# Kernel tuning notes

Measured on AMD Instinct MI355X. Metric: run time of the kernel, lower is better.

Reference implementation:

```python
import jax, jax.numpy as jnp
import numpy as np

D_MODEL = 1024
NUM_HEADS = 16
D_K = D_MODEL // NUM_HEADS
SCALE = float(np.sqrt(D_K))
NEG_FILL = -10000.0


def setup_inputs() -> dict:
    key = jax.random.key(0)
    ks = jax.random.split(key, 12)
    B, S = 2, 2048
    q = jax.random.normal(ks[0], (B, S, D_MODEL), dtype=jnp.float32)
    k = jax.random.normal(ks[1], (B, S, D_MODEL), dtype=jnp.float32)
    v = jax.random.normal(ks[2], (B, S, D_MODEL), dtype=jnp.float32)
    mask = jnp.ones((B, S, S), dtype=bool)
    w = lambda kk: jax.random.normal(kk, (D_MODEL, D_MODEL), dtype=jnp.float32) * 0.02
    b = lambda kk: jax.random.normal(kk, (D_MODEL,), dtype=jnp.float32) * 0.02
    return {
        "q": q, "k": k, "v": v, "mask": mask,
        "Wq": w(ks[3]), "bq": b(ks[4]),
        "Wk": w(ks[5]), "bk": b(ks[6]),
        "Wv": w(ks[7]), "bv": b(ks[8]),
        "Wo": w(ks[9]), "bo": b(ks[10]),
    }


def _mha(q, k, v, mask, Wq, bq, Wk, bk, Wv, bv, Wo, bo):
    B, S, _ = q.shape
    # torch Linear: x @ W.T + b
    def proj(x, W, bias):
        y = x @ W.T + bias
        return y.reshape(B, -1, NUM_HEADS, D_K).transpose(0, 2, 1, 3)  # [B,H,S,d_k]
    qh = proj(q, Wq, bq)
    kh = proj(k, Wk, bk)
    vh = proj(v, Wv, bv)
    scores = jnp.einsum('bhqd,bhkd->bhqk', qh, kh) / SCALE  # [B,H,S,S]
    scores = jnp.where(mask[:, None, :, :], scores, NEG_FILL)
    attn = jax.nn.softmax(scores, axis=-1)
    # dropout p=0.0 (eval) -> identity
    out = jnp.einsum('bhqk,bhkd->bhqd', attn, vh)  # [B,H,S,d_k]
    out = out.transpose(0, 2, 1, 3).reshape(B, -1, D_MODEL)
    return out @ Wo.T + bo


def reference(q, k, v, mask, Wq, bq, Wk, bk, Wv, bv, Wo, bo):
    return _mha(q, k, v, mask, Wq, bq, Wk, bk, Wv, bv, Wo, bo)
```

## Files before the change

kernel.cpp:

```cpp
#include <hip/hip_runtime.h>
#include <hip/hip_bf16.h>
#include <stdint.h>


typedef __bf16 bf16x8 __attribute__((ext_vector_type(8)));
typedef float  f32x4  __attribute__((ext_vector_type(4)));

#define GLD16(gp, lp)                                                         \
  __builtin_amdgcn_global_load_lds(                                           \
      (const __attribute__((address_space(1))) void*)(gp),                    \
      (__attribute__((address_space(3))) void*)(lp), 16, 0, 0)

#if __has_builtin(__builtin_amdgcn_exp2f)
#define EXP2F(x) __builtin_amdgcn_exp2f(x)
#else
#define EXP2F(x) exp2f(x)
#endif

__device__ __forceinline__ unsigned short f2bu(float f) {
  __bf16 b = (__bf16)f;
  return __builtin_bit_cast(unsigned short, b);
}
__device__ __forceinline__ f32x4 mfma16(bf16x8 a, bf16x8 b, f32x4 c) {
  return __builtin_amdgcn_mfma_f32_16x16x32_bf16(a, b, c, 0, 0, 0);
}

template <int CTRL>
__device__ __forceinline__ float dppf(float x) {
  int r = __builtin_amdgcn_update_dpp(0, __builtin_bit_cast(int, x),
                                      CTRL, 0xF, 0xF, true);
  return __builtin_bit_cast(float, r);
}
__device__ __forceinline__ float rowmax16(float x) {
  x = fmaxf(x, dppf<0xB1>(x));
  x = fmaxf(x, dppf<0x4E>(x));
  x = fmaxf(x, dppf<0x124>(x));
  x = fmaxf(x, dppf<0x128>(x));
  return x;
}
__device__ __forceinline__ float rowsum16(float x) {
  x += dppf<0xB1>(x);
  x += dppf<0x4E>(x);
  x += dppf<0x124>(x);
  x += dppf<0x128>(x);
  return x;
}

#define Q_PRESCALE 0.18033688011117290f
#define RESCALE_THR 8.0f

__global__ __launch_bounds__(256) void convert_kernel(
    const float* __restrict__ q, const float* __restrict__ k,
    const float* __restrict__ v, const float* __restrict__ wq,
    const float* __restrict__ wk, const float* __restrict__ wv,
    const float* __restrict__ wo, unsigned short* __restrict__ xq,
    unsigned short* __restrict__ xk, unsigned short* __restrict__ xv,
    unsigned short* __restrict__ cwq, unsigned short* __restrict__ cwk,
    unsigned short* __restrict__ cwv, unsigned short* __restrict__ cwo) {
  const int seg = blockIdx.y;
  const float* src; unsigned short* dst; int n4;
  const int NB = 4194304 / 4, NW = 1048576 / 4;
  switch (seg) {
    case 0: src = q;  dst = xq;  n4 = NB; break;
    case 1: src = k;  dst = xk;  n4 = NB; break;
    case 2: src = v;  dst = xv;  n4 = NB; break;
    case 3: src = wq; dst = cwq; n4 = NW; break;
    case 4: src = wk; dst = cwk; n4 = NW; break;
    case 5: src = wv; dst = cwv; n4 = NW; break;
    default: src = wo; dst = cwo; n4 = NW; break;
  }
  const int stride = gridDim.x * blockDim.x;
  for (int i = blockIdx.x * blockDim.x + threadIdx.x; i < n4; i += stride) {
    float4 f = ((const float4*)src)[i];
    ushort4 o;
    o.x = f2bu(f.x); o.y = f2bu(f.y); o.z = f2bu(f.z); o.w = f2bu(f.w);
    ((ushort4*)dst)[i] = o;
  }
}

template <int FN>
__device__ __forceinline__ void gemm_tile_bt(
    const unsigned short* __restrict__ A, const unsigned short* __restrict__ B,
    int am0, int bn0, unsigned short* sA, unsigned short* sB,
    f32x4 (&acc)[4][FN]) {
  const int tid = threadIdx.x;
  const int l = tid & 63, w = tid >> 6;
  const int wr = w >> 1, wc = w & 1;
  const f32x4 z4 = {0.f, 0.f, 0.f, 0.f};
#pragma unroll
  for (int i = 0; i < 4; i++)
#pragma unroll
    for (int j = 0; j < FN; j++) acc[i][j] = z4;

  for (int kk = 0; kk < 1024; kk += 64) {
#pragma unroll
    for (int it = 0; it < 4; ++it) {
      int c = it * 256 + tid;
      int row = c >> 3, c8 = (c & 7) * 8;
      GLD16(A + (size_t)(am0 + row) * 1024 + kk + c8,
            sA + (size_t)(it * 256 + w * 64) * 8);
    }
#pragma unroll
    for (int it = 0; it < FN; ++it) {
      int c = it * 256 + tid;
      int row = c >> 3, c8 = (c & 7) * 8;
      GLD16(B + (size_t)(bn0 + row) * 1024 + kk + c8,
            sB + (size_t)(it * 256 + w * 64) * 8);
    }
    __syncthreads();
    bf16x8 af[4][2], bfr[FN][2];
#pragma unroll
    for (int fm = 0; fm < 4; fm++)
#pragma unroll
      for (int h = 0; h < 2; h++)
        af[fm][h] = *reinterpret_cast<const bf16x8*>(
            sA + (wr * 64 + fm * 16 + (l & 15)) * 64 + 8 * (l >> 4) + 32 * h);
#pragma unroll
    for (int fn = 0; fn < FN; fn++)
#pragma unroll
      for (int h = 0; h < 2; h++)
        bfr[fn][h] = *reinterpret_cast<const bf16x8*>(
            sB + (wc * (FN * 16) + fn * 16 + (l & 15)) * 64 + 8 * (l >> 4) +
            32 * h);
#pragma unroll
    for (int fm = 0; fm < 4; fm++)
#pragma unroll
      for (int fn = 0; fn < FN; fn++) {
        acc[fm][fn] = mfma16(af[fm][0], bfr[fn][0], acc[fm][fn]);
        acc[fm][fn] = mfma16(af[fm][1], bfr[fn][1], acc[fm][fn]);
      }
    __syncthreads();
  }
}

__global__ __launch_bounds__(256, 3) void gemm_proj(
    const unsigned short* __restrict__ Xq, const unsigned short* __restrict__ Xk,
    const unsigned short* __restrict__ Xv, const unsigned short* __restrict__ Wq,
    const unsigned short* __restrict__ Wk, const unsigned short* __restrict__ Wv,
    const float* __restrict__ bq, const float* __restrict__ bk,
    const float* __restrict__ bv, unsigned short* __restrict__ Qh,
    unsigned short* __restrict__ Kh, unsigned short* __restrict__ Vt) {
  __shared__ unsigned short sA[128 * 64], sB[128 * 64];
  const int z = blockIdx.z;
  const unsigned short* X = (z == 0) ? Xq : (z == 1) ? Xk : Xv;
  const unsigned short* W = (z == 0) ? Wq : (z == 1) ? Wk : Wv;
  const float* bias = (z == 0) ? bq : (z == 1) ? bk : bv;
  const float scale = (z == 0) ? Q_PRESCALE : 1.0f;
  const int am0 = blockIdx.x * 128, bn0 = blockIdx.y * 128;
  f32x4 acc[4][4];
  gemm_tile_bt<4>(X, W, am0, bn0, sA, sB, acc);
  const int l = threadIdx.x & 63, w = threadIdx.x >> 6;
  const int wr = w >> 1, wc = w & 1;
  if (z < 2) {
    unsigned short* out = (z == 0) ? Qh : Kh;
#pragma unroll
    for (int fm = 0; fm < 4; fm++)
#pragma unroll
      for (int fn = 0; fn < 4; fn++) {
        int n = bn0 + wc * 64 + fn * 16 + (l & 15);
        int hh = n >> 6, d = n & 63;
        float bb = bias[n];
#pragma unroll
        for (int r = 0; r < 4; r++) {
          int m = am0 + wr * 64 + fm * 16 + (l >> 4) * 4 + r;
          int bidx = m >> 11, s = m & 2047;
          out[(((size_t)(bidx * 16 + hh) * 2048 + s)) * 64 + d] =
              f2bu((acc[fm][fn][r] + bb) * scale);
        }
      }
  } else {
#pragma unroll
    for (int fm = 0; fm < 4; fm++)
#pragma unroll
      for (int fn = 0; fn < 4; fn++) {
        int n = bn0 + wc * 64 + fn * 16 + (l & 15);
        int hh = n >> 6, d = n & 63;
        float bb = bias[n];
        int m0 = am0 + wr * 64 + fm * 16 + (l >> 4) * 4;
        int bidx = m0 >> 11, s0 = m0 & 2047;
        ushort4 pk;
        pk.x = f2bu(acc[fm][fn][0] + bb);
        pk.y = f2bu(acc[fm][fn][1] + bb);
        pk.z = f2bu(acc[fm][fn][2] + bb);
        pk.w = f2bu(acc[fm][fn][3] + bb);
        *(ushort4*)(Vt + ((size_t)(bidx * 16 + hh) * 64 + d) * 2048 + s0) = pk;
      }
  }
}

__global__ __launch_bounds__(256, 4) void attn_kernel(
    const unsigned short* __restrict__ Qh, const unsigned short* __restrict__ Kh,
    const unsigned short* __restrict__ Vt, unsigned short* __restrict__ Oh) {
  __shared__ unsigned short Ks[2][64 * 64];
  __shared__ unsigned short Vs[2][64 * 64];
  __shared__ unsigned short Ps[4][16 * 64];
  const int tid = threadIdx.x, l = tid & 63, w = tid >> 6;
  const int lid = blockIdx.x + 32 * blockIdx.y + 512 * blockIdx.z;
  const int swz = (lid & 7) * 128 + (lid >> 3);
  const int qt = swz & 31, h = (swz >> 5) & 15, b = swz >> 9;
  const size_t headoff = ((size_t)b * 16 + h) * 2048 * 64;
  const unsigned short* Qg = Qh + headoff + (size_t)(qt * 64 + w * 16) * 64;
  const unsigned short* Kg = Kh + headoff;
  const unsigned short* Vg = Vt + headoff;
  unsigned short* Pw = &Ps[w][0];

  bf16x8 qf[2];
#pragma unroll
  for (int hh = 0; hh < 2; hh++)
    qf[hh] = *reinterpret_cast<const bf16x8*>(
        Qg + (l & 15) * 64 + 8 * (l >> 4) + 32 * hh);

  float mrow[4], lrow[4];
  f32x4 oacc[4];
  const f32x4 z4 = {0.f, 0.f, 0.f, 0.f};
#pragma unroll
  for (int r = 0; r < 4; r++) { mrow[r] = -1e30f; lrow[r] = 0.f; }
#pragma unroll
  for (int fn = 0; fn < 4; fn++) oacc[fn] = z4;

  const int xoro[2] = { (((l >> 4) + 0) ^ (l & 7)) * 8,
                        (((l >> 4) + 4) ^ (l & 7)) * 8 };
  const int rowb = (l & 15) * 64;

#define STAGE_KV(dst, kt_)                                                    \
  do {                                                                        \
    _Pragma("unroll")                                                         \
    for (int it = 0; it < 2; ++it) {                                          \
      int c = it * 256 + tid;                                                 \
      int row = c >> 3;                                                       \
      int sc = (((c & 7) ^ (row & 7)) * 8);                                   \
      GLD16(Kg + (size_t)((kt_) * 64 + row) * 64 + sc,                        \
            &Ks[dst][0] + (size_t)(it * 256 + w * 64) * 8);                   \
      GLD16(Vg + (size_t)row * 2048 + (kt_) * 64 + sc,                        \
            &Vs[dst][0] + (size_t)(it * 256 + w * 64) * 8);                   \
    }                                                                         \
  } while (0)

  STAGE_KV(0, 0);
  __syncthreads();

#pragma unroll 2
  for (int kt = 0; kt < 32; ++kt) {
    const int cur = kt & 1;
    if (kt + 1 < 32) STAGE_KV(cur ^ 1, kt + 1);

    bf16x8 kf[4][2];
#pragma unroll
    for (int fn = 0; fn < 4; fn++)
#pragma unroll
      for (int hh = 0; hh < 2; hh++)
        kf[fn][hh] = *reinterpret_cast<const bf16x8*>(
            &Ks[cur][0] + fn * 1024 + rowb + xoro[hh]);
    f32x4 sfr[4];
#pragma unroll
    for (int fn = 0; fn < 4; fn++) {
      f32x4 sc = z4;
      sc = mfma16(qf[0], kf[fn][0], sc);
      sc = mfma16(qf[1], kf[fn][1], sc);
      sfr[fn] = sc;
    }

    float tmv[4];
    bool needb = false;
#pragma unroll
    for (int r = 0; r < 4; r++) {
      float tm = fmaxf(fmaxf(sfr[0][r], sfr[1][r]),
                       fmaxf(sfr[2][r], sfr[3][r]));
      tm = rowmax16(tm);
      tmv[r] = tm;
      needb = needb || (tm > mrow[r] + RESCALE_THR);
    }
    if (__any(needb)) {
#pragma unroll
      for (int r = 0; r < 4; r++) {
        float newm = fmaxf(mrow[r], tmv[r]);
        float corr = EXP2F(mrow[r] - newm);
        mrow[r] = newm;
        float rs = 0.f;
#pragma unroll
        for (int fn = 0; fn < 4; fn++) {
          float p = EXP2F(sfr[fn][r] - newm);
          sfr[fn][r] = p;
          rs += p;
        }
        rs = rowsum16(rs);
        lrow[r] = lrow[r] * corr + rs;
#pragma unroll
        for (int fn = 0; fn < 4; fn++) oacc[fn][r] *= corr;
      }
    } else {
#pragma unroll
      for (int r = 0; r < 4; r++) {
        float rs = 0.f;
#pragma unroll
        for (int fn = 0; fn < 4; fn++) {
          float p = EXP2F(sfr[fn][r] - mrow[r]);
          sfr[fn][r] = p;
          rs += p;
        }
        rs = rowsum16(rs);
        lrow[r] += rs;
      }
    }

    unsigned int pk[4][4];
#pragma unroll
    for (int fn = 0; fn < 4; fn++)
#pragma unroll
      for (int r = 0; r < 4; r++) {
        float p = sfr[fn][r];
        float po = dppf<0xB1>(p);
        pk[fn][r] = ((unsigned int)f2bu(po) << 16) | (unsigned int)f2bu(p);
      }
    if ((l & 1) == 0) {
      int qbase = (l >> 4) * 4, key0 = l & 15;
#pragma unroll
      for (int fn = 0; fn < 4; fn++)
#pragma unroll
        for (int r = 0; r < 4; r++) {
          int qr = qbase + r;
          int col = (fn * 16 + key0) ^ ((qr & 7) << 3);
          *(unsigned int*)(Pw + qr * 64 + col) = pk[fn][r];
        }
    }

    bf16x8 pf[2], vf[4][2];
#pragma unroll
    for (int hh = 0; hh < 2; hh++)
      pf[hh] = *reinterpret_cast<const bf16x8*>(Pw + rowb + xoro[hh]);
#pragma unroll
    for (int fn = 0; fn < 4; fn++)
#pragma unroll
      for (int hh = 0; hh < 2; hh++)
        vf[fn][hh] = *reinterpret_cast<const bf16x8*>(
            &Vs[cur][0] + fn * 1024 + rowb + xoro[hh]);
#pragma unroll
    for (int fn = 0; fn < 4; fn++) {
      oacc[fn] = mfma16(pf[0], vf[fn][0], oacc[fn]);
      oacc[fn] = mfma16(pf[1], vf[fn][1], oacc[fn]);
    }
    __syncthreads();
  }

  float inv[4];
#pragma unroll
  for (int r = 0; r < 4; r++) inv[r] = 1.0f / lrow[r];
#pragma unroll
  for (int fn = 0; fn < 4; fn++)
#pragma unroll
    for (int r = 0; r < 4; r++) {
      int qg = qt * 64 + w * 16 + (l >> 4) * 4 + r;
      int d = h * 64 + fn * 16 + (l & 15);
      Oh[((size_t)b * 2048 + qg) * 1024 + d] = f2bu(oacc[fn][r] * inv[r]);
    }
#undef STAGE_KV
}

__global__ __launch_bounds__(256, 3) void gemm_final(
    const unsigned short* __restrict__ O, const unsigned short* __restrict__ Wo,
    const float* __restrict__ bo, float* __restrict__ out) {
  __shared__ unsigned short sA[128 * 64], sB[64 * 64];
  const int am0 = blockIdx.x * 128, bn0 = blockIdx.y * 64;
  f32x4 acc[4][2];
  gemm_tile_bt<2>(O, Wo, am0, bn0, sA, sB, acc);
  const int l = threadIdx.x & 63, w = threadIdx.x >> 6;
  const int wr = w >> 1, wc = w & 1;
#pragma unroll
  for (int fm = 0; fm < 4; fm++)
#pragma unroll
    for (int fn = 0; fn < 2; fn++) {
      int n = bn0 + wc * 32 + fn * 16 + (l & 15);
      float bb = bo[n];
#pragma unroll
      for (int r = 0; r < 4; r++) {
        int m = am0 + wr * 64 + fm * 16 + (l >> 4) * 4 + r;
        out[(size_t)m * 1024 + n] = acc[fm][fn][r] + bb;
      }
    }
}

extern "C" void kernel_launch(void* const* d_in, const int* in_sizes, int n_in,
                              void* d_out, int out_size, void* d_ws,
                              size_t ws_size, hipStream_t stream) {
  (void)in_sizes; (void)n_in; (void)out_size; (void)ws_size;
  const float* q  = (const float*)d_in[0];
  const float* k  = (const float*)d_in[1];
  const float* v  = (const float*)d_in[2];
  const float* Wq = (const float*)d_in[4];
  const float* bq = (const float*)d_in[5];
  const float* Wk = (const float*)d_in[6];
  const float* bk = (const float*)d_in[7];
  const float* Wv = (const float*)d_in[8];
  const float* bv = (const float*)d_in[9];
  const float* Wo = (const float*)d_in[10];
  const float* bo = (const float*)d_in[11];
  float* out = (float*)d_out;
  char* ws = (char*)d_ws;

  unsigned short* Xq  = (unsigned short*)(ws);
  unsigned short* Xk  = (unsigned short*)(ws + 8388608);
  unsigned short* Xv  = (unsigned short*)(ws + 16777216);
  unsigned short* cWq = (unsigned short*)(ws + 25165824);
  unsigned short* cWk = (unsigned short*)(ws + 27262976);
  unsigned short* cWv = (unsigned short*)(ws + 29360128);
  unsigned short* cWo = (unsigned short*)(ws + 31457280);
  unsigned short* Qh  = (unsigned short*)(ws + 33554432);
  unsigned short* Kh  = (unsigned short*)(ws + 41943040);
  unsigned short* Vt  = (unsigned short*)(ws + 50331648);
  unsigned short* Oh  = (unsigned short*)(ws);

  convert_kernel<<<dim3(1024, 7, 1), 256, 0, stream>>>(
      q, k, v, Wq, Wk, Wv, Wo, Xq, Xk, Xv, cWq, cWk, cWv, cWo);
  gemm_proj<<<dim3(32, 8, 3), 256, 0, stream>>>(
      Xq, Xk, Xv, cWq, cWk, cWv, bq, bk, bv, Qh, Kh, Vt);
  attn_kernel<<<dim3(32, 16, 2), 256, 0, stream>>>(Qh, Kh, Vt, Oh);
  gemm_final<<<dim3(32, 16, 1), 256, 0, stream>>>(Oh, cWo, bo, out);
}
```

Measured before the change: 282.2 us.

## Compute softmax row sums via MFMA with ones and defer row-max reduction

The per-tile softmax denominator is now accumulated by extra MFMAs of the bf16 P fragments against a ones vector, replacing the DPP row-sum reductions. The cross-lane row-max reduction runs only on the rescale path; the threshold check uses each lane's partial max instead. The change also adds s_setprio around the MFMA blocks and a packed bf16 convert instruction. It trades VALU and DPP work for two extra MFMAs per tile, and the denominator is now summed from bf16-rounded probabilities.

```diff
diff --git a/kernel.cpp b/kernel.cpp
--- a/kernel.cpp
+++ b/kernel.cpp
@@ -36,13 +36,6 @@
   x = fmaxf(x, dppf<0x4E>(x));
   x = fmaxf(x, dppf<0x124>(x));
   x = fmaxf(x, dppf<0x128>(x));
-  return x;
-}
-__device__ __forceinline__ float rowsum16(float x) {
-  x += dppf<0xB1>(x);
-  x += dppf<0x4E>(x);
-  x += dppf<0x124>(x);
-  x += dppf<0x128>(x);
   return x;
 }
 
@@ -210,13 +203,19 @@
     qf[hh] = *reinterpret_cast<const bf16x8*>(
         Qg + (l & 15) * 64 + 8 * (l >> 4) + 32 * hh);
 
-  float mrow[4], lrow[4];
-  f32x4 oacc[4];
+  bf16x8 onesf;
+#pragma unroll
+  for (int i = 0; i < 8; i++)
+    onesf[i] = __builtin_bit_cast(__bf16, (unsigned short)0x3F80);
+
+  float mrow[4];
+  f32x4 oacc[4], lacc;
   const f32x4 z4 = {0.f, 0.f, 0.f, 0.f};
 #pragma unroll
-  for (int r = 0; r < 4; r++) { mrow[r] = -1e30f; lrow[r] = 0.f; }
+  for (int r = 0; r < 4; r++) mrow[r] = -1e30f;
 #pragma unroll
   for (int fn = 0; fn < 4; fn++) oacc[fn] = z4;
+  lacc = z4;
 
   const int xoro[2] = { (((l >> 4) + 0) ^ (l & 7)) * 8,
                         (((l >> 4) + 4) ^ (l & 7)) * 8 };
@@ -252,6 +251,7 @@
         kf[fn][hh] = *reinterpret_cast<const bf16x8*>(
             &Ks[cur][0] + fn * 1024 + rowb + xoro[hh]);
     f32x4 sfr[4];
+    __builtin_amdgcn_s_setprio(1);
 #pragma unroll
     for (int fn = 0; fn < 4; fn++) {
       f32x4 sc = z4;
@@ -259,6 +259,7 @@
       sc = mfma16(qf[1], kf[fn][1], sc);
       sfr[fn] = sc;
     }
+    __builtin_amdgcn_s_setprio(0);
 
     float tmv[4];
     bool needb = false;
@@ -266,41 +267,29 @@
     for (int r = 0; r < 4; r++) {
       float tm = fmaxf(fmaxf(sfr[0][r], sfr[1][r]),
                        fmaxf(sfr[2][r], sfr[3][r]));
-      tm = rowmax16(tm);
       tmv[r] = tm;
       needb = needb || (tm > mrow[r] + RESCALE_THR);
     }
     if (__any(needb)) {
 #pragma unroll
       for (int r = 0; r < 4; r++) {
-        float newm = fmaxf(mrow[r], tmv[r]);
+        float tm = rowmax16(tmv[r]);
+        float newm = fmaxf(mrow[r], tm);
         float corr = EXP2F(mrow[r] - newm);
         mrow[r] = newm;
-        float rs = 0.f;
-#pragma unroll
-        for (int fn = 0; fn < 4; fn++) {
-          float p = EXP2F(sfr[fn][r] - newm);
-          sfr[fn][r] = p;
-          rs += p;
-        }
-        rs = rowsum16(rs);
-        lrow[r] = lrow[r] * corr + rs;
+#pragma unroll
+        for (int fn = 0; fn < 4; fn++)
+          sfr[fn][r] = EXP2F(sfr[fn][r] - newm);
+        lacc[r] *= corr;
 #pragma unroll
         for (int fn = 0; fn < 4; fn++) oacc[fn][r] *= corr;
       }
     } else {
 #pragma unroll
-      for (int r = 0; r < 4; r++) {
-        float rs = 0.f;
-#pragma unroll
-        for (int fn = 0; fn < 4; fn++) {
-          float p = EXP2F(sfr[fn][r] - mrow[r]);
-          sfr[fn][r] = p;
-          rs += p;
-        }
-        rs = rowsum16(rs);
-        lrow[r] += rs;
-      }
+      for (int r = 0; r < 4; r++)
+#pragma unroll
+        for (int fn = 0; fn < 4; fn++)
+          sfr[fn][r] = EXP2F(sfr[fn][r] - mrow[r]);
     }
 
     unsigned int pk[4][4];
@@ -310,7 +299,9 @@
       for (int r = 0; r < 4; r++) {
         float p = sfr[fn][r];
         float po = dppf<0xB1>(p);
-        pk[fn][r] = ((unsigned int)f2bu(po) << 16) | (unsigned int)f2bu(p);
+        unsigned int d;
+        asm("v_cvt_pk_bf16_f32 %0, %1, %2" : "=v"(d) : "v"(p), "v"(po));
+        pk[fn][r] = d;
       }
     if ((l & 1) == 0) {
       int qbase = (l >> 4) * 4, key0 = l & 15;
@@ -334,17 +325,21 @@
       for (int hh = 0; hh < 2; hh++)
         vf[fn][hh] = *reinterpret_cast<const bf16x8*>(
             &Vs[cur][0] + fn * 1024 + rowb + xoro[hh]);
+    __builtin_amdgcn_s_setprio(1);
 #pragma unroll
     for (int fn = 0; fn < 4; fn++) {
       oacc[fn] = mfma16(pf[0], vf[fn][0], oacc[fn]);
       oacc[fn] = mfma16(pf[1], vf[fn][1], oacc[fn]);
     }
+    lacc = mfma16(pf[0], onesf, lacc);
+    lacc = mfma16(pf[1], onesf, lacc);
+    __builtin_amdgcn_s_setprio(0);
     __syncthreads();
   }
 
   float inv[4];
 #pragma unroll
-  for (int r = 0; r < 4; r++) inv[r] = 1.0f / lrow[r];
+  for (int r = 0; r < 4; r++) inv[r] = 1.0f / lacc[r];
 #pragma unroll
   for (int fn = 0; fn < 4; fn++)
 #pragma unroll
```

Result: faster. 262.7 us (-6.9%).
